# Performance work log

Measured on AMD Instinct MI355X. Metric: run time of the kernel, lower is better.

## Reference

```python
import jax, jax.numpy as jnp
import numpy as np

DAMPENING = 50.0
THR = 1.0
TAU = 10.0
DECAY = float(np.exp(-1.0 / TAU))
V_MIN = -1.0


@jax.custom_vjp
def spike_fn(v_scaled):
    # Heaviside spike with surrogate (triangular) gradient
    return (v_scaled > 0.0).astype(v_scaled.dtype)

def _spike_fwd(v_scaled):
    return spike_fn(v_scaled), v_scaled

def _spike_bwd(v_scaled, dy):
    return (dy * DAMPENING * jnp.maximum(0.0, 1.0 - jnp.abs(v_scaled)),)

spike_fn.defvjp(_spike_fwd, _spike_bwd)


def setup_inputs() -> dict:
    key = jax.random.key(0)
    T, B, N_IN, N = 256, 32, 256, 2048
    ks = jax.random.split(key, 4)
    x = jax.random.normal(ks[0], (T, B, N_IN), jnp.float32)
    W_in = jax.random.normal(ks[1], (N_IN, N), jnp.float32) * (1.0 / np.sqrt(N_IN))
    b = jnp.zeros((N,), jnp.float32)
    # original uses stddev 1/sqrt(n_in) for Bernoulli_weights as well
    W_bern = jax.random.normal(ks[2], (N, N), jnp.float32) * (1.0 / np.sqrt(N_IN))
    random_indices = jax.random.randint(ks[3], (T, N), 0, N)
    return {"x": x, "W_in": W_in, "b": b, "W_bern": W_bern,
            "random_indices": random_indices}


def reference(x, W_in, b, W_bern, random_indices):
    # x: [T, B, n_in]; states v, z2: [B, n]
    B, N = x.shape[1], W_in.shape[1]
    v0 = jnp.zeros((B, N), x.dtype)
    z2_0 = jnp.zeros((B, N), x.dtype)  # old_spike state (unused in math, as in original)

    def step(carry, inp):
        v, _old_z2 = carry
        xt, idx = inp
        i_in = xt @ W_in + b                               # [B, n]
        new_v = jnp.clip(DECAY * v + i_in, V_MIN, THR + 0.01)
        z = spike_fn(new_v - THR)                          # spikes [B, n]
        new_v = jnp.where(z > 0.0, V_MIN, new_v)           # hard reset
        z2 = jnp.take(z @ W_bern, idx, axis=1)             # stochastic projection + column gather
        return (new_v, z2), (z, new_v, z2)

    _, (zs, vs, z2s) = jax.lax.scan(step, (v0, z2_0), (x, random_indices))
    return jnp.stack([zs, vs, z2s], axis=0)  # [3, T, B, n]
```

## Files before the change

### kernel.cpp

```cpp
#include <hip/hip_runtime.h>
#include <hip/hip_bf16.h>
#include <stdint.h>


#define T_STEPS 256
#define BATCH   32
#define NIN     256
#define NN      2048
#define BN_FLAT (BATCH * NN)
#define TBN     (T_STEPS * BATCH * NN)
#define MROWS   (T_STEPS * BATCH)

typedef __attribute__((ext_vector_type(4))) float fx4;
typedef __attribute__((ext_vector_type(4))) int   ix4;

__device__ __forceinline__ void gll16(const void* g, void* l) {
  typedef __attribute__((address_space(1))) void gvoid_t;
  typedef __attribute__((address_space(3))) void lvoid_t;
  __builtin_amdgcn_global_load_lds((gvoid_t*)(g), (lvoid_t*)(l), 16, 0, 0);
}

__device__ __forceinline__ void mfma16(fx4& d, ix4 a, ix4 b) {
  asm volatile("v_mfma_f32_16x16x32_bf16 %0, %1, %2, %0" : "+v"(d) : "v"(a), "v"(b));
}

__global__ __launch_bounds__(256) void wt_convert(const float* __restrict__ W,
                                                  __hip_bfloat16* __restrict__ Wt) {
  __shared__ float tile[32][33];
  const int k0 = blockIdx.y << 5, n0 = blockIdx.x << 5;
  const int tx = threadIdx.x, ty = threadIdx.y;
#pragma unroll
  for (int i = 0; i < 32; i += 8)
    tile[ty + i][tx] = W[(size_t)(k0 + ty + i) * NN + n0 + tx];
  __syncthreads();
#pragma unroll
  for (int i = 0; i < 32; i += 8)
    Wt[(size_t)(n0 + ty + i) * NN + k0 + tx] = __float2bfloat16(tile[tx][ty + i]);
}

__global__ __launch_bounds__(256) void in_gemm(const float* __restrict__ X,
                                               const float* __restrict__ Wi,
                                               const float* __restrict__ bias,
                                               float* __restrict__ I) {
  __shared__ float As[16][68];
  __shared__ float Bs[16][64];
  const int tid = threadIdx.x;
  const int tx = tid & 15, ty = tid >> 4;
  const int m0 = blockIdx.x * 64, n0 = blockIdx.y * 64;
  float acc[4][4] = {};
  for (int k0 = 0; k0 < NIN; k0 += 16) {
#pragma unroll
    for (int it = 0; it < 4; ++it) {
      int r = (tid >> 4) + it * 16;
      As[tid & 15][r] = X[(size_t)(m0 + r) * NIN + k0 + (tid & 15)];
    }
#pragma unroll
    for (int it = 0; it < 4; ++it) {
      int kk = (tid >> 6) + it * 4;
      int c = tid & 63;
      Bs[kk][c] = Wi[(size_t)(k0 + kk) * NN + n0 + c];
    }
    __syncthreads();
#pragma unroll
    for (int kk = 0; kk < 16; ++kk) {
      fx4 a = *(const fx4*)&As[kk][ty * 4];
      fx4 b = *(const fx4*)&Bs[kk][tx * 4];
#pragma unroll
      for (int i = 0; i < 4; ++i)
#pragma unroll
        for (int j = 0; j < 4; ++j)
          acc[i][j] = fmaf(a[i], b[j], acc[i][j]);
    }
    __syncthreads();
  }
#pragma unroll
  for (int i = 0; i < 4; ++i) {
    int r = m0 + ty * 4 + i;
    fx4 res;
#pragma unroll
    for (int j = 0; j < 4; ++j) res[j] = acc[i][j] + bias[n0 + tx * 4 + j];
    *(fx4*)&I[(size_t)r * NN + n0 + tx * 4] = res;
  }
}

__device__ __forceinline__ void scan_body(float* zs, float* vsout,
                                          const float* I, __hip_bfloat16* Zb) {
  const int nid = blockIdx.x * 256 + threadIdx.x;
  float v = 0.f;
  for (int t0 = 0; t0 < T_STEPS; t0 += 8) {
    float iin[8];
#pragma unroll
    for (int u = 0; u < 8; ++u)
      iin[u] = I[(size_t)(t0 + u) * BN_FLAT + nid];
#pragma unroll
    for (int u = 0; u < 8; ++u) {
      float nv = __fadd_rn(__fmul_rn(0.9048374180359595f, v), iin[u]);
      nv = fminf(fmaxf(nv, -1.0f), 1.01f);
      const bool sp = nv > 1.0f;
      const float z = sp ? 1.0f : 0.0f;
      nv = sp ? -1.0f : nv;
      const size_t off = (size_t)(t0 + u) * BN_FLAT + nid;
      zs[off] = z;
      vsout[off] = nv;
      Zb[off] = __float2bfloat16(z);
      v = nv;
    }
  }
}

__global__ __launch_bounds__(256) void scan_sep(float* __restrict__ out,
                                                const float* __restrict__ I,
                                                __hip_bfloat16* __restrict__ Zb) {
  scan_body(out, out + (size_t)TBN, I, Zb);
}

__global__ __launch_bounds__(256) void scan_inp(float* out, __hip_bfloat16* Zb) {
  scan_body(out, out + (size_t)TBN, out + (size_t)TBN, Zb);
}

__global__ __launch_bounds__(256) void bern_gemm(const __hip_bfloat16* __restrict__ Z,
                                                 const __hip_bfloat16* __restrict__ Wt,
                                                 float* __restrict__ Y) {
  __shared__ __align__(16) __hip_bfloat16 Asm[128 * 32];
  __shared__ __align__(16) __hip_bfloat16 Bsm[128 * 32];
  const int tid = threadIdx.x;
  const int lane = tid & 63;
  const int wid = tid >> 6;
  const int wr = wid >> 1, wc = wid & 1;
  const int m0 = blockIdx.x * 128, n0 = blockIdx.y * 128;

  fx4 acc[4][4] = {};

  const int trow = tid >> 2;
  const int tcol = (tid & 3) << 4;
  const char* gA = (const char*)Z + ((size_t)(m0 + trow) << 12) + tcol;
  const char* gB = (const char*)Wt + ((size_t)(n0 + trow) << 12) + tcol;
  char* lA = (char*)Asm + tid * 16;
  char* lB = (char*)Bsm + tid * 16;

  const ix4* Au = (const ix4*)Asm;
  const ix4* Bu = (const ix4*)Bsm;
  const int abase = (wr * 64 + (lane & 15)) * 4 + (lane >> 4);
  const int bbase = (wc * 64 + (lane & 15)) * 4 + (lane >> 4);

  for (int ks = 0; ks < 64; ++ks) {
    gll16(gA, lA);
    gll16(gA + (size_t)64 * 4096, lA + 4096);
    gll16(gB, lB);
    gll16(gB + (size_t)64 * 4096, lB + 4096);
    gA += 64;
    gB += 64;
    __syncthreads();

    ix4 af[4], bf[4];
#pragma unroll
    for (int i = 0; i < 4; ++i) af[i] = Au[abase + i * 64];
#pragma unroll
    for (int i = 0; i < 4; ++i) bf[i] = Bu[bbase + i * 64];
#pragma unroll
    for (int mf = 0; mf < 4; ++mf)
#pragma unroll
      for (int nf = 0; nf < 4; ++nf)
        mfma16(acc[mf][nf], af[mf], bf[nf]);
    __syncthreads();
  }

  asm volatile("s_nop 7\n\ts_nop 7");

  const int crow = (lane >> 4) * 4;
  const int ccol = lane & 15;
#pragma unroll
  for (int mf = 0; mf < 4; ++mf)
#pragma unroll
    for (int nf = 0; nf < 4; ++nf)
#pragma unroll
      for (int j = 0; j < 4; ++j) {
        const int r = m0 + wr * 64 + mf * 16 + crow + j;
        const int c = n0 + wc * 64 + nf * 16 + ccol;
        Y[(size_t)r * NN + c] = acc[mf][nf][j];
      }
}

__global__ __launch_bounds__(256) void gather_k(float* __restrict__ Y,
                                                const int* __restrict__ ridx) {
  __shared__ __align__(16) float rowbuf[NN];
  const int tb = blockIdx.x;
  const int t = tb >> 5;
  float* yrow = Y + (size_t)tb * NN;
  const int tid = threadIdx.x;
#pragma unroll
  for (int i = 0; i < 2; ++i) {
    int u = tid + i * 256;
    ((fx4*)rowbuf)[u] = ((const fx4*)yrow)[u];
  }
  __syncthreads();
  const int* ir = ridx + t * NN;
#pragma unroll
  for (int i = 0; i < 8; ++i) {
    int j = tid + i * 256;
    yrow[j] = rowbuf[ir[j]];
  }
}

extern "C" void kernel_launch(void* const* d_in, const int* in_sizes, int n_in,
                              void* d_out, int out_size, void* d_ws, size_t ws_size,
                              hipStream_t stream) {
  const float* x      = (const float*)d_in[0];
  const float* W_in   = (const float*)d_in[1];
  const float* bias   = (const float*)d_in[2];
  const float* W_bern = (const float*)d_in[3];
  const int*   ridx   = (const int*)d_in[4];
  float* out = (float*)d_out;
  char* ws = (char*)d_ws;

  __hip_bfloat16* Wt = (__hip_bfloat16*)ws;
  __hip_bfloat16* Zb = (__hip_bfloat16*)(ws + (size_t)8388608);
  const size_t offI = 41943040;
  const bool sep = ws_size >= (size_t)109051904;
  float* Ibuf = sep ? (float*)(ws + offI) : (out + (size_t)TBN);

  wt_convert<<<dim3(64, 64), dim3(32, 8), 0, stream>>>(W_bern, Wt);
  in_gemm<<<dim3(128, 32), dim3(256), 0, stream>>>(x, W_in, bias, Ibuf);
  if (sep)
    scan_sep<<<dim3(256), dim3(256), 0, stream>>>(out, Ibuf, Zb);
  else
    scan_inp<<<dim3(256), dim3(256), 0, stream>>>(out, Zb);
  bern_gemm<<<dim3(64, 16), dim3(256), 0, stream>>>(Zb, Wt, out + (size_t)2 * TBN);
  gather_k<<<dim3(8192), dim3(256), 0, stream>>>(out + (size_t)2 * TBN, ridx);
}
```

Before: 263.4 us.

## Pre-transpose X and enlarge input GEMM tiles with direct-to-LDS loads

Adds a kernel that transposes x into a K-major scratch buffer placed in the output region. The fp32 input GEMM is rewritten with 256x128 block tiles, 16x8 register microtiles, and global_load_lds transfers, replacing the 64x64 tiles and strided scalar loads. The goal is more arithmetic per shared-memory and global load, plus coalesced A loads. The cost is an extra launch and transpose pass, heavy register pressure from 128 accumulators per thread, and fewer blocks (512) to fill the GPU.

```diff
diff --git a/kernel.cpp b/kernel.cpp
--- a/kernel.cpp
+++ b/kernel.cpp
@@ -24,6 +24,20 @@
   asm volatile("v_mfma_f32_16x16x32_bf16 %0, %1, %2, %0" : "+v"(d) : "v"(a), "v"(b));
 }
 
+__global__ __launch_bounds__(256) void xt_k(const float* __restrict__ X,
+                                            float* __restrict__ Xt) {
+  __shared__ float tile[32][33];
+  const int m0 = blockIdx.x << 5, k0 = blockIdx.y << 5;
+  const int tx = threadIdx.x, ty = threadIdx.y;
+#pragma unroll
+  for (int i = 0; i < 32; i += 8)
+    tile[ty + i][tx] = X[(size_t)(m0 + ty + i) * NIN + k0 + tx];
+  __syncthreads();
+#pragma unroll
+  for (int i = 0; i < 32; i += 8)
+    Xt[(size_t)(k0 + ty + i) * MROWS + m0 + tx] = tile[tx][ty + i];
+}
+
 __global__ __launch_bounds__(256) void wt_convert(const float* __restrict__ W,
                                                   __hip_bfloat16* __restrict__ Wt) {
   __shared__ float tile[32][33];
@@ -38,48 +52,65 @@
     Wt[(size_t)(n0 + ty + i) * NN + k0 + tx] = __float2bfloat16(tile[tx][ty + i]);
 }
 
-__global__ __launch_bounds__(256) void in_gemm(const float* __restrict__ X,
-                                               const float* __restrict__ Wi,
-                                               const float* __restrict__ bias,
-                                               float* __restrict__ I) {
-  __shared__ float As[16][68];
-  __shared__ float Bs[16][64];
+__global__ __launch_bounds__(256, 2) void in_gemm(const float* __restrict__ Xt,
+                                                  const float* __restrict__ Wi,
+                                                  const float* __restrict__ bias,
+                                                  float* __restrict__ I) {
+  __shared__ __align__(16) float As[16 * 256];
+  __shared__ __align__(16) float Bs[16 * 128];
   const int tid = threadIdx.x;
-  const int tx = tid & 15, ty = tid >> 4;
-  const int m0 = blockIdx.x * 64, n0 = blockIdx.y * 64;
-  float acc[4][4] = {};
+  const int lane = tid & 63;
+  const int w = tid >> 6;
+  const int tm = tid >> 4;
+  const int tn = tid & 15;
+  const int m0 = blockIdx.x * 256, n0 = blockIdx.y * 128;
+
+  fx4 acc[16][2] = {};
+
+  const char* gA = (const char*)(Xt + (size_t)(w * 4) * MROWS + m0 + lane * 4);
+  char* lA = (char*)As + w * 4096 + lane * 16;
+  const char* gB = (const char*)(Wi + (size_t)(w * 4 + (lane >> 5)) * NN + n0 + (lane & 31) * 4);
+  char* lB = (char*)Bs + w * 2048 + lane * 16;
+
   for (int k0 = 0; k0 < NIN; k0 += 16) {
 #pragma unroll
-    for (int it = 0; it < 4; ++it) {
-      int r = (tid >> 4) + it * 16;
-      As[tid & 15][r] = X[(size_t)(m0 + r) * NIN + k0 + (tid & 15)];
+    for (int i = 0; i < 4; ++i) gll16(gA + (size_t)i * (MROWS * 4), lA + i * 1024);
+#pragma unroll
+    for (int j = 0; j < 2; ++j) gll16(gB + (size_t)j * (2 * NN * 4), lB + j * 1024);
+    gA += (size_t)16 * MROWS * 4;
+    gB += (size_t)16 * NN * 4;
+    __syncthreads();
+#pragma unroll
+    for (int kk = 0; kk < 16; ++kk) {
+      fx4 av[4], bv[2];
+#pragma unroll
+      for (int q = 0; q < 4; ++q) av[q] = *(const fx4*)&As[kk * 256 + tm * 16 + q * 4];
+      bv[0] = *(const fx4*)&Bs[kk * 128 + tn * 4];
+      bv[1] = *(const fx4*)&Bs[kk * 128 + 64 + tn * 4];
+#pragma unroll
+      for (int r = 0; r < 16; ++r) {
+        const float a = av[r >> 2][r & 3];
+#pragma unroll
+        for (int j = 0; j < 2; ++j)
+#pragma unroll
+          for (int c = 0; c < 4; ++c)
+            acc[r][j][c] = fmaf(a, bv[j][c], acc[r][j][c]);
+      }
     }
-#pragma unroll
-    for (int it = 0; it < 4; ++it) {
-      int kk = (tid >> 6) + it * 4;
-      int c = tid & 63;
-      Bs[kk][c] = Wi[(size_t)(k0 + kk) * NN + n0 + c];
+    __syncthreads();
+  }
+
+#pragma unroll
+  for (int r = 0; r < 16; ++r) {
+    const size_t row = (size_t)(m0 + tm * 16 + r) * NN;
+    fx4 r0, r1;
+#pragma unroll
+    for (int c = 0; c < 4; ++c) {
+      r0[c] = acc[r][0][c] + bias[n0 + tn * 4 + c];
+      r1[c] = acc[r][1][c] + bias[n0 + 64 + tn * 4 + c];
     }
-    __syncthreads();
-#pragma unroll
-    for (int kk = 0; kk < 16; ++kk) {
-      fx4 a = *(const fx4*)&As[kk][ty * 4];
-      fx4 b = *(const fx4*)&Bs[kk][tx * 4];
-#pragma unroll
-      for (int i = 0; i < 4; ++i)
-#pragma unroll
-        for (int j = 0; j < 4; ++j)
-          acc[i][j] = fmaf(a[i], b[j], acc[i][j]);
-    }
-    __syncthreads();
-  }
-#pragma unroll
-  for (int i = 0; i < 4; ++i) {
-    int r = m0 + ty * 4 + i;
-    fx4 res;
-#pragma unroll
-    for (int j = 0; j < 4; ++j) res[j] = acc[i][j] + bias[n0 + tx * 4 + j];
-    *(fx4*)&I[(size_t)r * NN + n0 + tx * 4] = res;
+    *(fx4*)&I[row + n0 + tn * 4] = r0;
+    *(fx4*)&I[row + n0 + 64 + tn * 4] = r1;
   }
 }
 
@@ -219,8 +250,11 @@
   const bool sep = ws_size >= (size_t)109051904;
   float* Ibuf = sep ? (float*)(ws + offI) : (out + (size_t)TBN);
 
+  float* Xt = out;
+
+  xt_k<<<dim3(256, 8), dim3(32, 8), 0, stream>>>(x, Xt);
   wt_convert<<<dim3(64, 64), dim3(32, 8), 0, stream>>>(W_bern, Wt);
-  in_gemm<<<dim3(128, 32), dim3(256), 0, stream>>>(x, W_in, bias, Ibuf);
+  in_gemm<<<dim3(32, 16), dim3(256), 0, stream>>>(Xt, W_in, bias, Ibuf);
   if (sep)
     scan_sep<<<dim3(256), dim3(256), 0, stream>>>(out, Ibuf, Zb);
   else
```

Result: faster. 252.3 us (-4.2%).
